# Kernel optimization log

Hardware: AMD Instinct MI355X
Metric: run time of the kernel (lower is better)

The kernel has to match this reference:

```python
import jax, jax.numpy as jnp
import numpy as np

NUM_ITEMS = 1_000_000
EMBED_DIM = 128
BATCH, SEQ = 16, 256
NUM_NEG = 256
TEMP = 0.05
EPS = 1e-12


def _l2norm(x):
    # F.normalize(p=2, dim=-1) with eps=1e-12
    n = jnp.sqrt(jnp.sum(x * x, axis=-1, keepdims=True))
    return x / jnp.maximum(n, EPS)


def setup_inputs() -> dict:
    key = jax.random.key(0)
    k1, k2, k3, k4, k5, k6 = jax.random.split(key, 6)
    output_embeddings = jax.random.normal(k1, (BATCH, SEQ, EMBED_DIM), jnp.float32)
    all_item_embeddings = jax.random.normal(k2, (NUM_ITEMS + 1, EMBED_DIM), jnp.float32)
    target_ids = jax.random.randint(k3, (BATCH, SEQ), 1, NUM_ITEMS + 1, jnp.int32)
    w = jax.random.uniform(k4, (BATCH, SEQ), jnp.float32)
    supervision_weights = jnp.where(w > 0.2, w, 0.0)
    N = BATCH * SEQ
    # negatives sampled uniformly in [1, num_items]; resample once on collision with target
    neg1 = jax.random.randint(k5, (N, NUM_NEG), 1, NUM_ITEMS + 1, jnp.int32)
    neg2 = jax.random.randint(k6, (N, NUM_NEG), 1, NUM_ITEMS + 1, jnp.int32)
    flat_t = target_ids.reshape(-1)
    neg_item_ids = jnp.where(neg1 != flat_t[:, None], neg1, neg2)
    return {
        "output_embeddings": output_embeddings,
        "all_item_embeddings": all_item_embeddings,
        "supervision_weights": supervision_weights,
        "target_ids": target_ids,
        "neg_item_ids": neg_item_ids,
    }


def reference(output_embeddings, all_item_embeddings, supervision_weights,
              target_ids, neg_item_ids):
    B, S, D = output_embeddings.shape
    max_item_idx = all_item_embeddings.shape[0] - 1  # = num_items

    flat_out = output_embeddings.reshape(-1, D)           # [N, D]
    flat_t = target_ids.reshape(-1)                       # [N]
    flat_w = supervision_weights.reshape(-1)              # [N]

    # instead of compacting valid rows, compute everywhere and weight by w
    # (w == 0 on invalid rows, so the weighted mean is identical)
    tgt_idx = jnp.clip(flat_t - 1, 0, max_item_idx)       # [N]

    q = _l2norm(flat_out)                                  # [N, D]
    norm_table = _l2norm(all_item_embeddings)              # full-table normalize (faithful)

    pos_emb = norm_table[tgt_idx]                          # [N, D]
    pos_logits = jnp.sum(q * pos_emb, axis=1, keepdims=True)  # [N, 1]

    neg_idx = jnp.clip(neg_item_ids - 1, 0, max_item_idx)  # [N, K]
    neg_emb = norm_table[neg_idx]                          # [N, K, D]
    neg_logits = jnp.einsum('nd,nkd->nk', q, neg_emb)      # [N, K]

    logits = jnp.concatenate([pos_logits, neg_logits], axis=1) / TEMP  # [N, 1+K]
    # cross-entropy with label 0
    loss_per = jax.nn.logsumexp(logits, axis=1) - logits[:, 0]          # [N]

    return jnp.sum(loss_per * flat_w) / jnp.sum(flat_w)
```

## Files before the change

### kernel.cpp

```cpp
#include <hip/hip_runtime.h>
#include <math.h>

#define DIMS 128
#define KNEG 256
#define INV_TEMP 20.0f
#define EPSN 1e-12f

__global__ __launch_bounds__(256) void ssl_row_kernel(
    const float* __restrict__ out_emb,
    const float* __restrict__ table,
    const float* __restrict__ w,
    const int*   __restrict__ tgt,
    const int*   __restrict__ negs,
    float*       __restrict__ loss_out,
    int max_row)
{
    const int n = blockIdx.x;
    const int t = threadIdx.x;

    __shared__ __align__(16) float q_lds[DIMS];
    __shared__ float logits[KNEG + 1];
    __shared__ int   nid[KNEG];
    __shared__ float red[8];

    const float wn = w[n];
    if (wn == 0.0f) {
        if (t == 0) loss_out[n] = 0.0f;
        return;
    }

    float x = 0.0f;
    if (t < DIMS) x = out_emb[(size_t)n * DIMS + t];
    float ss = x * x;
    #pragma unroll
    for (int m = 1; m < 64; m <<= 1) ss += __shfl_xor(ss, m, 64);
    if ((t & 63) == 0) red[t >> 6] = ss;
    if (t < KNEG) nid[t] = negs[(size_t)n * KNEG + t];
    __syncthreads();
    const float inv_qn = 1.0f / fmaxf(sqrtf(red[0] + red[1]), EPSN);
    if (t < DIMS) q_lds[t] = x * inv_qn;
    __syncthreads();

    const int hw   = t >> 5;
    const int lane = t & 31;
    const float4 qv = *(const float4*)(q_lds + lane * 4);
    const int tgtn = tgt[n];

    #pragma unroll 1
    for (int k = 0; k < 32; k += 2) {
        const int j1 = hw + (k << 3);
        const int j2 = j1 + 8;
        int id1 = (j1 == 0) ? tgtn : nid[j1 - 1];
        int id2 = nid[j2 - 1];
        int i1 = id1 - 1; i1 = i1 < 0 ? 0 : (i1 > max_row ? max_row : i1);
        int i2 = id2 - 1; i2 = i2 < 0 ? 0 : (i2 > max_row ? max_row : i2);
        const float4 e1 = ((const float4*)(table + (size_t)i1 * DIMS))[lane];
        const float4 e2 = ((const float4*)(table + (size_t)i2 * DIMS))[lane];
        float dq1 = qv.x*e1.x + qv.y*e1.y + qv.z*e1.z + qv.w*e1.w;
        float de1 = e1.x*e1.x + e1.y*e1.y + e1.z*e1.z + e1.w*e1.w;
        float dq2 = qv.x*e2.x + qv.y*e2.y + qv.z*e2.z + qv.w*e2.w;
        float de2 = e2.x*e2.x + e2.y*e2.y + e2.z*e2.z + e2.w*e2.w;
        #pragma unroll
        for (int m = 1; m < 32; m <<= 1) {
            dq1 += __shfl_xor(dq1, m, 64);
            de1 += __shfl_xor(de1, m, 64);
            dq2 += __shfl_xor(dq2, m, 64);
            de2 += __shfl_xor(de2, m, 64);
        }
        if (lane == 0) {
            logits[j1] = dq1 / fmaxf(sqrtf(de1), EPSN) * INV_TEMP;
            logits[j2] = dq2 / fmaxf(sqrtf(de2), EPSN) * INV_TEMP;
        }
    }
    if (hw == 0) {
        int id = nid[KNEG - 1];
        int i1 = id - 1; i1 = i1 < 0 ? 0 : (i1 > max_row ? max_row : i1);
        const float4 e1 = ((const float4*)(table + (size_t)i1 * DIMS))[lane];
        float dq1 = qv.x*e1.x + qv.y*e1.y + qv.z*e1.z + qv.w*e1.w;
        float de1 = e1.x*e1.x + e1.y*e1.y + e1.z*e1.z + e1.w*e1.w;
        #pragma unroll
        for (int m = 1; m < 32; m <<= 1) {
            dq1 += __shfl_xor(dq1, m, 64);
            de1 += __shfl_xor(de1, m, 64);
        }
        if (lane == 0) logits[KNEG] = dq1 / fmaxf(sqrtf(de1), EPSN) * INV_TEMP;
    }
    __syncthreads();

    float mx = logits[t];
    if (t == 0) mx = fmaxf(mx, logits[KNEG]);
    #pragma unroll
    for (int m = 1; m < 64; m <<= 1) mx = fmaxf(mx, __shfl_xor(mx, m, 64));
    if ((t & 63) == 0) red[t >> 6] = mx;
    __syncthreads();
    if (t == 0) red[4] = fmaxf(fmaxf(red[0], red[1]), fmaxf(red[2], red[3]));
    __syncthreads();
    mx = red[4];

    float p = expf(logits[t] - mx);
    if (t == 0) p += expf(logits[KNEG] - mx);
    #pragma unroll
    for (int m = 1; m < 64; m <<= 1) p += __shfl_xor(p, m, 64);
    if ((t & 63) == 0) red[t >> 6] = p;
    __syncthreads();
    if (t == 0) {
        const float s   = red[0] + red[1] + red[2] + red[3];
        const float lse = mx + logf(s);
        loss_out[n] = (lse - logits[0]) * wn;
    }
}

__global__ __launch_bounds__(256) void ssl_reduce_kernel(
    const float* __restrict__ loss,
    const float* __restrict__ w,
    float* __restrict__ out, int n)
{
    __shared__ float red[8];
    const int t = threadIdx.x;
    float sl = 0.0f, sw = 0.0f;
    for (int i = t; i < n; i += 256) { sl += loss[i]; sw += w[i]; }
    #pragma unroll
    for (int m = 1; m < 64; m <<= 1) {
        sl += __shfl_xor(sl, m, 64);
        sw += __shfl_xor(sw, m, 64);
    }
    if ((t & 63) == 0) { red[t >> 6] = sl; red[4 + (t >> 6)] = sw; }
    __syncthreads();
    if (t == 0) {
        const float SL = red[0] + red[1] + red[2] + red[3];
        const float SW = red[4] + red[5] + red[6] + red[7];
        out[0] = SL / SW;
    }
}

extern "C" void kernel_launch(void* const* d_in, const int* in_sizes, int n_in,
                              void* d_out, int out_size, void* d_ws, size_t ws_size,
                              hipStream_t stream) {
    const float* out_emb = (const float*)d_in[0];
    const float* table   = (const float*)d_in[1];
    const float* w       = (const float*)d_in[2];
    const int*   tgt     = (const int*)d_in[3];
    const int*   negs    = (const int*)d_in[4];

    const int N = in_sizes[2];
    const int rows = in_sizes[1] / DIMS;
    const int max_row = rows - 1;

    float* loss_ws = (float*)d_ws;

    ssl_row_kernel<<<N, 256, 0, stream>>>(out_emb, table, w, tgt, negs, loss_ws, max_row);
    ssl_reduce_kernel<<<1, 256, 0, stream>>>(loss_ws, w, (float*)d_out, N);
}
```

Before: 84.14 us.

## Process two rows per block and partition gathers into table-range passes

Each block now handles two query rows, and the 257 gathered item rows are fetched in three passes, each restricted to one third of the table index range. The goal is to make concurrently running blocks touch the same slice of the 512 MB table at roughly the same time, improving L2/MALL locality. The dot and norm shuffle reductions are also merged to share shuffle steps. The cost is repeated scanning of the index lists, divergent predicated loads, and a grid half the size, and passes are not synchronized across blocks, so the locality gain may not appear.

After: 133.1 us. 1.58x slower.

```diff
diff --git a/kernel.cpp b/kernel.cpp
--- a/kernel.cpp
+++ b/kernel.cpp
@@ -5,108 +5,121 @@
 #define KNEG 256
 #define INV_TEMP 20.0f
 #define EPSN 1e-12f
+#define PASSES 3
 
-__global__ __launch_bounds__(256) void ssl_row_kernel(
+__global__ __launch_bounds__(256, 8) void ssl_row_kernel(
     const float* __restrict__ out_emb,
     const float* __restrict__ table,
     const float* __restrict__ w,
     const int*   __restrict__ tgt,
     const int*   __restrict__ negs,
     float*       __restrict__ loss_out,
-    int max_row)
+    int N, int max_row)
 {
-    const int n = blockIdx.x;
-    const int t = threadIdx.x;
+    const int t    = threadIdx.x;
+    const int hw   = t >> 5;
+    const int lane = t & 31;
+    const int n0   = blockIdx.x;
+    const int n1   = blockIdx.x + (N >> 1);
 
-    __shared__ __align__(16) float q_lds[DIMS];
-    __shared__ float logits[KNEG + 1];
-    __shared__ int   nid[KNEG];
+    __shared__ __align__(16) float q_lds[2][DIMS];
+    __shared__ float logits[2][KNEG + 1];
+    __shared__ int   nid[2][KNEG];
     __shared__ float red[8];
 
-    const float wn = w[n];
-    if (wn == 0.0f) {
-        if (t == 0) loss_out[n] = 0.0f;
-        return;
+    const float w0 = w[n0], w1 = w[n1];
+    const bool  v0 = (w0 != 0.0f), v1 = (w1 != 0.0f);
+    if (t == 0) {
+        if (!v0) loss_out[n0] = 0.0f;
+        if (!v1) loss_out[n1] = 0.0f;
+    }
+    if (!v0 && !v1) return;
+
+    {
+        const int r  = t >> 7;
+        const int d  = t & 127;
+        const int nr = r ? n1 : n0;
+        const float x = out_emb[(size_t)nr * DIMS + d];
+        float ss = x * x;
+        #pragma unroll
+        for (int m = 1; m < 64; m <<= 1) ss += __shfl_xor(ss, m, 64);
+        if ((t & 63) == 0) red[t >> 6] = ss;
+        nid[0][t] = negs[(size_t)n0 * KNEG + t];
+        nid[1][t] = negs[(size_t)n1 * KNEG + t];
+        __syncthreads();
+        const float inv = 1.0f / fmaxf(sqrtf(red[2 * r] + red[2 * r + 1]), EPSN);
+        q_lds[r][d] = x * inv;
+        __syncthreads();
     }
 
-    float x = 0.0f;
-    if (t < DIMS) x = out_emb[(size_t)n * DIMS + t];
-    float ss = x * x;
-    #pragma unroll
-    for (int m = 1; m < 64; m <<= 1) ss += __shfl_xor(ss, m, 64);
-    if ((t & 63) == 0) red[t >> 6] = ss;
-    if (t < KNEG) nid[t] = negs[(size_t)n * KNEG + t];
-    __syncthreads();
-    const float inv_qn = 1.0f / fmaxf(sqrtf(red[0] + red[1]), EPSN);
-    if (t < DIMS) q_lds[t] = x * inv_qn;
-    __syncthreads();
+    const float4 qv0 = *(const float4*)(&q_lds[0][lane * 4]);
+    const float4 qv1 = *(const float4*)(&q_lds[1][lane * 4]);
+    const int tgt0 = tgt[n0], tgt1 = tgt[n1];
+    const long long M = (long long)max_row + 1;
 
-    const int hw   = t >> 5;
-    const int lane = t & 31;
-    const float4 qv = *(const float4*)(q_lds + lane * 4);
-    const int tgtn = tgt[n];
+    auto do_elem = [&](int r, int idx, int j, const float4& qv) {
+        const float4 e = ((const float4*)(table + (size_t)idx * DIMS))[lane];
+        float dq = qv.x*e.x + qv.y*e.y + qv.z*e.z + qv.w*e.w;
+        float de = e.x*e.x + e.y*e.y + e.z*e.z + e.w*e.w;
+        dq += __shfl_xor(dq, 16, 64); de += __shfl_xor(de, 16, 64);
+        dq += __shfl_xor(dq, 8, 64);  de += __shfl_xor(de, 8, 64);
+        float v = (lane & 8) ? de : dq;
+        v += __shfl_xor(v, 1, 64);
+        v += __shfl_xor(v, 2, 64);
+        v += __shfl_xor(v, 4, 64);
+        const float u = __shfl_xor(v, 8, 64);
+        if (lane == 0) logits[r][j] = v / fmaxf(sqrtf(u), EPSN) * INV_TEMP;
+    };
 
-    #pragma unroll 1
-    for (int k = 0; k < 32; k += 2) {
-        const int j1 = hw + (k << 3);
-        const int j2 = j1 + 8;
-        int id1 = (j1 == 0) ? tgtn : nid[j1 - 1];
-        int id2 = nid[j2 - 1];
-        int i1 = id1 - 1; i1 = i1 < 0 ? 0 : (i1 > max_row ? max_row : i1);
-        int i2 = id2 - 1; i2 = i2 < 0 ? 0 : (i2 > max_row ? max_row : i2);
-        const float4 e1 = ((const float4*)(table + (size_t)i1 * DIMS))[lane];
-        const float4 e2 = ((const float4*)(table + (size_t)i2 * DIMS))[lane];
-        float dq1 = qv.x*e1.x + qv.y*e1.y + qv.z*e1.z + qv.w*e1.w;
-        float de1 = e1.x*e1.x + e1.y*e1.y + e1.z*e1.z + e1.w*e1.w;
-        float dq2 = qv.x*e2.x + qv.y*e2.y + qv.z*e2.z + qv.w*e2.w;
-        float de2 = e2.x*e2.x + e2.y*e2.y + e2.z*e2.z + e2.w*e2.w;
-        #pragma unroll
-        for (int m = 1; m < 32; m <<= 1) {
-            dq1 += __shfl_xor(dq1, m, 64);
-            de1 += __shfl_xor(de1, m, 64);
-            dq2 += __shfl_xor(dq2, m, 64);
-            de2 += __shfl_xor(de2, m, 64);
+    for (int pass = 0; pass < PASSES; ++pass) {
+        const int lo = (int)(( (long long)pass      * M) / PASSES);
+        const int hi = (int)(( (long long)(pass + 1)* M) / PASSES);
+        #pragma unroll 1
+        for (int r = 0; r < 2; ++r) {
+            if (r ? !v1 : !v0) continue;
+            const float4 qv = r ? qv1 : qv0;
+            const int tg = r ? tgt1 : tgt0;
+            #pragma unroll 4
+            for (int i = 0; i < 32; ++i) {
+                const int j  = (hw << 5) + i;
+                const int id = (j == 0) ? tg : nid[r][j - 1];
+                int idx = id - 1; idx = idx < 0 ? 0 : (idx > max_row ? max_row : idx);
+                if (idx >= lo && idx < hi) do_elem(r, idx, j, qv);
+            }
+            if (hw == 7) {
+                const int id = nid[r][KNEG - 1];
+                int idx = id - 1; idx = idx < 0 ? 0 : (idx > max_row ? max_row : idx);
+                if (idx >= lo && idx < hi) do_elem(r, idx, KNEG, qv);
+            }
         }
-        if (lane == 0) {
-            logits[j1] = dq1 / fmaxf(sqrtf(de1), EPSN) * INV_TEMP;
-            logits[j2] = dq2 / fmaxf(sqrtf(de2), EPSN) * INV_TEMP;
-        }
-    }
-    if (hw == 0) {
-        int id = nid[KNEG - 1];
-        int i1 = id - 1; i1 = i1 < 0 ? 0 : (i1 > max_row ? max_row : i1);
-        const float4 e1 = ((const float4*)(table + (size_t)i1 * DIMS))[lane];
-        float dq1 = qv.x*e1.x + qv.y*e1.y + qv.z*e1.z + qv.w*e1.w;
-        float de1 = e1.x*e1.x + e1.y*e1.y + e1.z*e1.z + e1.w*e1.w;
-        #pragma unroll
-        for (int m = 1; m < 32; m <<= 1) {
-            dq1 += __shfl_xor(dq1, m, 64);
-            de1 += __shfl_xor(de1, m, 64);
-        }
-        if (lane == 0) logits[KNEG] = dq1 / fmaxf(sqrtf(de1), EPSN) * INV_TEMP;
     }
     __syncthreads();
 
-    float mx = logits[t];
-    if (t == 0) mx = fmaxf(mx, logits[KNEG]);
-    #pragma unroll
-    for (int m = 1; m < 64; m <<= 1) mx = fmaxf(mx, __shfl_xor(mx, m, 64));
-    if ((t & 63) == 0) red[t >> 6] = mx;
-    __syncthreads();
-    if (t == 0) red[4] = fmaxf(fmaxf(red[0], red[1]), fmaxf(red[2], red[3]));
-    __syncthreads();
-    mx = red[4];
+    #pragma unroll 1
+    for (int r = 0; r < 2; ++r) {
+        if (r ? !v1 : !v0) continue;
+        float mx = logits[r][t];
+        if (t == 0) mx = fmaxf(mx, logits[r][KNEG]);
+        #pragma unroll
+        for (int m = 1; m < 64; m <<= 1) mx = fmaxf(mx, __shfl_xor(mx, m, 64));
+        if ((t & 63) == 0) red[t >> 6] = mx;
+        __syncthreads();
+        if (t == 0) red[4] = fmaxf(fmaxf(red[0], red[1]), fmaxf(red[2], red[3]));
+        __syncthreads();
+        mx = red[4];
 
-    float p = expf(logits[t] - mx);
-    if (t == 0) p += expf(logits[KNEG] - mx);
-    #pragma unroll
-    for (int m = 1; m < 64; m <<= 1) p += __shfl_xor(p, m, 64);
-    if ((t & 63) == 0) red[t >> 6] = p;
-    __syncthreads();
-    if (t == 0) {
-        const float s   = red[0] + red[1] + red[2] + red[3];
-        const float lse = mx + logf(s);
-        loss_out[n] = (lse - logits[0]) * wn;
+        float pp = expf(logits[r][t] - mx);
+        if (t == 0) pp += expf(logits[r][KNEG] - mx);
+        #pragma unroll
+        for (int m = 1; m < 64; m <<= 1) pp += __shfl_xor(pp, m, 64);
+        if ((t & 63) == 0) red[t >> 6] = pp;
+        __syncthreads();
+        if (t == 0) {
+            const float s   = red[0] + red[1] + red[2] + red[3];
+            const float lse = mx + logf(s);
+            loss_out[r ? n1 : n0] = (lse - logits[r][0]) * (r ? w1 : w0);
+        }
+        __syncthreads();
     }
 }
 
@@ -148,6 +161,7 @@
 
     float* loss_ws = (float*)d_ws;
 
-    ssl_row_kernel<<<N, 256, 0, stream>>>(out_emb, table, w, tgt, negs, loss_ws, max_row);
+    ssl_row_kernel<<<N / 2, 256, 0, stream>>>(out_emb, table, w, tgt, negs,
+                                              loss_ws, N, max_row);
     ssl_reduce_kernel<<<1, 256, 0, stream>>>(loss_ws, w, (float*)d_out, N);
 }
```
